# Kernel tuning notes

Hardware: AMD Instinct MI355X
Metric: run time of the kernel (lower is better)

The kernel has to match this reference:

```python
import jax, jax.numpy as jnp
import numpy as np

B, N, C = 1, 512, 256
LN_EPS = 1e-5


def mish(x):
    return x * jnp.tanh(jax.nn.softplus(x))


def layer_norm(x, g, b):
    mu = jnp.mean(x, axis=-1, keepdims=True)
    var = jnp.var(x, axis=-1, keepdims=True)
    return (x - mu) * jax.lax.rsqrt(var + LN_EPS) * g + b


def setup_inputs() -> dict:
    key = jax.random.key(0)
    ks = jax.random.split(key, 8)
    s = 1.0 / np.sqrt(C)
    lin = lambda k: jax.random.uniform(k, (C, C), jnp.float32, -s, s)
    return {
        "feat": jax.random.normal(ks[0], (B, N, C), jnp.float32),
        "Wq": lin(ks[1]), "bq": jnp.zeros((C,), jnp.float32),
        "ln_q_g": jnp.ones((C,), jnp.float32), "ln_q_b": jnp.zeros((C,), jnp.float32),
        "Wk": lin(ks[2]), "bk": jnp.zeros((C,), jnp.float32),
        "ln_k_g": jnp.ones((C,), jnp.float32), "ln_k_b": jnp.zeros((C,), jnp.float32),
        "Wv": lin(ks[3]), "bv": jnp.zeros((C,), jnp.float32),
        "W1": lin(ks[4]), "b1": jnp.zeros((C,), jnp.float32),
        "ln_w_g": jnp.ones((C,), jnp.float32), "ln_w_b": jnp.zeros((C,), jnp.float32),
        "W2": lin(ks[5]), "b2": jnp.zeros((C,), jnp.float32),
    }


def reference(feat, Wq, bq, ln_q_g, ln_q_b, Wk, bk, ln_k_g, ln_k_b,
              Wv, bv, W1, b1, ln_w_g, ln_w_b, W2, b2):
    # distribution: 1 where the row has any nonzero feature, else 0  -> [B, N, 1]
    dist = (jnp.sum(jnp.abs(feat), axis=-1, keepdims=True) > 0).astype(feat.dtype)

    q = mish(layer_norm(feat @ Wq + bq, ln_q_g, ln_q_b))  # [B, N, C]
    k = mish(layer_norm(feat @ Wk + bk, ln_k_g, ln_k_b))  # [B, N, C]
    v = feat @ Wv + bv                                     # [B, N, C]

    # relation_qk[b, i, j, c] = k[b, j, c] - q[b, i, c]
    rel = k[:, None, :, :] - q[:, :, None, :]              # [B, N, N, C]
    w = mish(layer_norm(rel @ W1 + b1, ln_w_g, ln_w_b)) @ W2 + b2  # [B, N, N, C]

    # weighted softmax over the key axis j (dim=-2), weights = dist -> [B,1,N,1]
    wts = dist[:, None, :, :]                              # [B, 1, N, 1]
    m = jnp.max(w, axis=-2, keepdims=True)
    e = jnp.exp(w - m) * wts
    attn = e / jnp.sum(e, axis=-2, keepdims=True)          # [B, N, N, C]

    mask = (dist * jnp.swapaxes(dist, -1, -2)) > 0         # [B, N, N]
    attn = attn * mask[..., None].astype(attn.dtype)

    return jnp.einsum('bijk,bjk->bik', attn, v)            # [B, N, C]
```

## Files before the change

### kernel.cpp

```cpp
#include <hip/hip_runtime.h>
#include <hip/hip_bf16.h>
#include <math.h>


#define N_ 512
#define C_ 256
#define NCHUNK 2
#define JPB (N_ / NCHUNK)
#define JT 32

typedef short s8v __attribute__((ext_vector_type(8)));
typedef short s4v __attribute__((ext_vector_type(4)));
typedef float f4v __attribute__((ext_vector_type(4)));
typedef float f16v __attribute__((ext_vector_type(16)));
typedef unsigned int u4v __attribute__((ext_vector_type(4)));

__device__ __forceinline__ unsigned short f2bf(float x) {
  union { __hip_bfloat16 h; unsigned short u; } cv;
  cv.h = __float2bfloat16(x);
  return cv.u;
}

__device__ __forceinline__ float mish_f(float x) {
  if (x > 25.f) return x;
  float y = 1.f + __expf(x);
  float y2 = y * y;
  return x * __fdividef(y2 - 1.f, y2 + 1.f);
}

__device__ __forceinline__ void blockReduce2(float& a, float& b, float* red) {
  #pragma unroll
  for (int m = 1; m < 64; m <<= 1) { a += __shfl_xor(a, m); b += __shfl_xor(b, m); }
  int lane = threadIdx.x & 63, w = threadIdx.x >> 6;
  if (lane == 0) { red[w] = a; red[4 + w] = b; }
  __syncthreads();
  a = red[0] + red[1] + red[2] + red[3];
  b = red[4] + red[5] + red[6] + red[7];
  __syncthreads();
}

__global__ void __launch_bounds__(256) prep_kernel(
    const float* __restrict__ feat,
    const float* __restrict__ Wq, const float* __restrict__ bq,
    const float* __restrict__ gq, const float* __restrict__ bgq,
    const float* __restrict__ Wk, const float* __restrict__ bk,
    const float* __restrict__ gk, const float* __restrict__ bgk,
    const float* __restrict__ Wv, const float* __restrict__ bv,
    const float* __restrict__ W1, const float* __restrict__ b1,
    float* __restrict__ dist, float* __restrict__ vout,
    float* __restrict__ Qp, float* __restrict__ Kp,
    float* __restrict__ muQ, float* __restrict__ s2Q,
    float* __restrict__ muK, float* __restrict__ s2K,
    unsigned short* __restrict__ Qb, unsigned short* __restrict__ Kb) {
  const int tid = threadIdx.x;
  const int r0 = blockIdx.x * 4;
  __shared__ float fL[4][C_];
  __shared__ float xq[4][C_];
  __shared__ float xk[4][C_];
  __shared__ float red[8];

  #pragma unroll
  for (int r = 0; r < 4; ++r) fL[r][tid] = feat[(r0 + r) * C_ + tid];
  __syncthreads();

  {
    float a = fabsf(fL[0][tid]), b = fabsf(fL[1][tid]);
    blockReduce2(a, b, red);
    if (tid == 0) { dist[r0 + 0] = a > 0.f ? 1.f : 0.f; dist[r0 + 1] = b > 0.f ? 1.f : 0.f; }
    a = fabsf(fL[2][tid]); b = fabsf(fL[3][tid]);
    blockReduce2(a, b, red);
    if (tid == 0) { dist[r0 + 2] = a > 0.f ? 1.f : 0.f; dist[r0 + 3] = b > 0.f ? 1.f : 0.f; }
  }

  float aq[4] = {0,0,0,0}, ak[4] = {0,0,0,0}, av[4] = {0,0,0,0};
  for (int cp = 0; cp < C_; ++cp) {
    float wq = Wq[cp * C_ + tid], wk = Wk[cp * C_ + tid], wv = Wv[cp * C_ + tid];
    #pragma unroll
    for (int r = 0; r < 4; ++r) {
      float f = fL[r][cp];
      aq[r] += f * wq; ak[r] += f * wk; av[r] += f * wv;
    }
  }
  {
    float bvv = bv[tid];
    #pragma unroll
    for (int r = 0; r < 4; ++r) vout[(r0 + r) * C_ + tid] = av[r] + bvv;
  }

  const float bqv = bq[tid], bkv = bk[tid];
  const float gqv = gq[tid], bgqv = bgq[tid], gkv = gk[tid], bgkv = bgk[tid];
  for (int r = 0; r < 4; ++r) {
    float qv = aq[r] + bqv, kv = ak[r] + bkv;
    float s1 = qv, s2 = qv * qv;
    blockReduce2(s1, s2, red);
    float mu = s1 * (1.f / C_);
    float rs = rsqrtf(s2 * (1.f / C_) - mu * mu + 1e-5f);
    xq[r][tid] = mish_f((qv - mu) * rs * gqv + bgqv);
    s1 = kv; s2 = kv * kv;
    blockReduce2(s1, s2, red);
    mu = s1 * (1.f / C_);
    rs = rsqrtf(s2 * (1.f / C_) - mu * mu + 1e-5f);
    xk[r][tid] = mish_f((kv - mu) * rs * gkv + bgkv);
  }
  __syncthreads();

  float pq[4] = {0,0,0,0}, pk[4] = {0,0,0,0};
  for (int cp = 0; cp < C_; ++cp) {
    float w1 = W1[cp * C_ + tid];
    #pragma unroll
    for (int r = 0; r < 4; ++r) { pq[r] += xq[r][cp] * w1; pk[r] += xk[r][cp] * w1; }
  }
  const float b1v = b1[tid];
  for (int r = 0; r < 4; ++r) {
    float qv2 = pq[r];
    float kv2 = pk[r] + b1v;
    Qp[(r0 + r) * C_ + tid] = qv2;
    Kp[(r0 + r) * C_ + tid] = kv2;
    Qb[(r0 + r) * C_ + tid] = f2bf(qv2);
    Kb[(r0 + r) * C_ + tid] = f2bf(kv2);
    float s1 = qv2, s2 = qv2 * qv2;
    blockReduce2(s1, s2, red);
    if (tid == 0) { muQ[r0 + r] = s1 * (1.f / C_); s2Q[r0 + r] = s2; }
    s1 = kv2; s2 = kv2 * kv2;
    blockReduce2(s1, s2, red);
    if (tid == 0) { muK[r0 + r] = s1 * (1.f / C_); s2K[r0 + r] = s2; }
  }
}

__global__ void __launch_bounds__(256) repack_kernel(
    const float* __restrict__ W2, unsigned short* __restrict__ W2f) {
  int idx = blockIdx.x * 256 + threadIdx.x;
  int e = idx & 7;
  int l = (idx >> 3) & 63;
  int ks = (idx >> 9) & 15;
  int w = idx >> 13;
  int k = ks * 16 + ((l >> 5) << 3) + e;
  int c = (w << 5) + (l & 31);
  W2f[idx] = f2bf(W2[k * C_ + c]);
}

__global__ void __launch_bounds__(256) gemmG_kernel(
    const unsigned short* __restrict__ Qb, const unsigned short* __restrict__ Kb,
    float* __restrict__ G) {
  const int tid = threadIdx.x;
  const int lane = tid & 63, wave = tid >> 6;
  const int bi = blockIdx.x >> 4, bj = blockIdx.x & 15;
  const int i0 = bi * 32 + (wave >> 1) * 16;
  const int j0 = bj * 32 + (wave & 1) * 16;
  const int jr = lane & 15, kg = lane >> 4;
  const unsigned short* qrow = Qb + (i0 + jr) * C_;
  const unsigned short* krow = Kb + (j0 + jr) * C_;
  f4v acc = (f4v){0.f, 0.f, 0.f, 0.f};
  #pragma unroll
  for (int ks = 0; ks < 8; ++ks) {
    const int kb = ks * 32 + kg * 4;
    s4v alo = *reinterpret_cast<const s4v*>(qrow + kb);
    s4v ahi = *reinterpret_cast<const s4v*>(qrow + kb + 16);
    s4v blo = *reinterpret_cast<const s4v*>(krow + kb);
    s4v bhi = *reinterpret_cast<const s4v*>(krow + kb + 16);
    s8v A, Bv;
    A[0]=alo[0];A[1]=alo[1];A[2]=alo[2];A[3]=alo[3];
    A[4]=ahi[0];A[5]=ahi[1];A[6]=ahi[2];A[7]=ahi[3];
    Bv[0]=blo[0];Bv[1]=blo[1];Bv[2]=blo[2];Bv[3]=blo[3];
    Bv[4]=bhi[0];Bv[5]=bhi[1];Bv[6]=bhi[2];Bv[7]=bhi[3];
    acc = __builtin_amdgcn_mfma_f32_16x16x32_bf16(A, Bv, acc, 0, 0, 0);
  }
  #pragma unroll
  for (int r = 0; r < 4; ++r)
    G[(i0 + kg * 4 + r) * N_ + j0 + jr] = acc[r];
}

__global__ void __launch_bounds__(512, 4) attn_kernel(
    const float* __restrict__ dist, const float* __restrict__ v,
    const float* __restrict__ Qp, const float* __restrict__ Kp,
    const float* __restrict__ muQ, const float* __restrict__ s2Q,
    const float* __restrict__ muK, const float* __restrict__ s2K,
    const float* __restrict__ G, const unsigned short* __restrict__ W2f,
    const float* __restrict__ gw, const float* __restrict__ bw,
    float* __restrict__ pden, float* __restrict__ pacc) {
  const int tid = threadIdx.x;
  const int i = blockIdx.x;
  const int chunk = blockIdx.y;
  const int j0 = chunk * JPB;
  const int lane = tid & 63, wave = tid >> 6;
  const int jg = tid >> 4, g = tid & 15;
  const int row = lane & 31, hi = lane >> 5;
  const int cw = (wave << 5) + row;

  __shared__ __align__(16) unsigned short T[JT * C_];
  __shared__ __align__(16) float qpP[80 * 4];
  __shared__ __align__(16) float gbL[144 * 4];
  __shared__ float muKL[JPB], s2KL[JPB], GL[JPB], distL[JPB];
  char* Tb = reinterpret_cast<char*>(T);

  if (tid < C_) {
    const int c = tid;
    qpP[(5 * (c >> 4) + ((c >> 2) & 3)) * 4 + (c & 3)] = Qp[i * C_ + c];
    const int pc = 9 * (c >> 4) + ((c & 15) >> 1);
    gbL[pc * 4 + (c & 1) * 2]     = gw[c];
    gbL[pc * 4 + (c & 1) * 2 + 1] = bw[c];
    muKL[tid] = muK[j0 + tid];
    s2KL[tid] = s2K[j0 + tid];
  } else {
    const int t = tid - C_;
    GL[t]    = G[i * N_ + j0 + t];
    distL[t] = dist[j0 + t];
  }

  s8v Bfr[16];
  #pragma unroll
  for (int ks = 0; ks < 16; ++ks)
    Bfr[ks] = *reinterpret_cast<const s8v*>(
        W2f + ((((wave << 4) + ks) * 64 + lane) << 3));

  const float muQ_i = muQ[i], s2Q_i = s2Q[i];

  float den = 0.f, accv = 0.f;
  __syncthreads();

  const int swz = (g & 7) << 6;
  const int wb0 = (((((g << 1)    ) << 5) + jg) << 4) ^ swz;
  const int wb1 = (((((g << 1) + 1) << 5) + jg) << 4) ^ swz;
  const f4v* qp4 = reinterpret_cast<const f4v*>(qpP) + 5 * g;
  const f4v* gb4 = reinterpret_cast<const f4v*>(gbL) + 9 * g;

  for (int jt = 0; jt < JPB / JT; ++jt) {
    const int jb = j0 + jt * JT;
    {
      const int jj = jt * JT + jg;
      const float muj = muKL[jj] - muQ_i;
      const float ex2 = (s2KL[jj] + s2Q_i - 2.f * GL[jj]) * (1.f / C_);
      const float rs = rsqrtf(fmaxf(ex2 - muj * muj, 0.f) + 1e-5f);
      const float* kpr = Kp + (j0 + jj) * C_ + (g << 4);
      u4v p0, p1;
      #pragma unroll
      for (int m = 0; m < 4; ++m) {
        f4v kk = *reinterpret_cast<const f4v*>(kpr + (m << 2));
        f4v qq = qp4[m];
        f4v ga  = gb4[2 * m];
        f4v gb_ = gb4[2 * m + 1];
        #pragma unroll
        for (int h = 0; h < 2; ++h) {
          f4v gg = h ? gb_ : ga;
          float x0 = kk[2 * h]     - qq[2 * h]     - muj;
          float x1 = kk[2 * h + 1] - qq[2 * h + 1] - muj;
          float a  = mish_f(fmaf(x0, rs * gg[0], gg[1]));
          float b2 = mish_f(fmaf(x1, rs * gg[2], gg[3]));
          unsigned pa = (__float_as_uint(a) + 0x8000u) >> 16;
          unsigned pb = (__float_as_uint(b2) + 0x8000u) & 0xFFFF0000u;
          unsigned pk = pa | pb;
          if (m < 2) p0[m * 2 + h] = pk; else p1[(m - 2) * 2 + h] = pk;
        }
      }
      *reinterpret_cast<u4v*>(Tb + wb0) = p0;
      *reinterpret_cast<u4v*>(Tb + wb1) = p1;
    }
    __syncthreads();

    f16v wv;
    #pragma unroll
    for (int r = 0; r < 16; ++r) wv[r] = 0.f;
    #pragma unroll
    for (int ks = 0; ks < 16; ++ks) {
      const int off = (((((ks << 1) + hi) << 5) + row) << 4) ^ ((ks & 7) << 6);
      s8v A = *reinterpret_cast<const s8v*>(Tb + off);
      wv = __builtin_amdgcn_mfma_f32_32x32x16_bf16(A, Bfr[ks], wv, 0, 0, 0);
    }

    #pragma unroll
    for (int r = 0; r < 16; ++r) {
      const int jj = (r & 3) + ((r >> 2) << 3) + (hi << 2);
      float e = __expf(fminf(wv[r], 60.f)) * distL[jt * JT + jj];
      den += e;
      accv += e * v[(jb + jj) * C_ + cw];
    }
    __syncthreads();
  }

  den  += __shfl_xor(den, 32);
  accv += __shfl_xor(accv, 32);
  if (lane < 32) {
    pden[(chunk * N_ + i) * C_ + cw] = den;
    pacc[(chunk * N_ + i) * C_ + cw] = accv;
  }
}

__global__ void __launch_bounds__(256) reduce_kernel(
    const float* __restrict__ dist,
    const float* __restrict__ pden, const float* __restrict__ pacc,
    float* __restrict__ out) {
  const int i = blockIdx.x, c = threadIdx.x;
  float den = 0.f, acc = 0.f;
  #pragma unroll
  for (int ch = 0; ch < NCHUNK; ++ch) {
    den += pden[(ch * N_ + i) * C_ + c];
    acc += pacc[(ch * N_ + i) * C_ + c];
  }
  float o = 0.f;
  if (dist[i] > 0.f && den > 0.f) o = acc / den;
  out[i * C_ + c] = o;
}

extern "C" void kernel_launch(void* const* d_in, const int* in_sizes, int n_in,
                              void* d_out, int out_size, void* d_ws, size_t ws_size,
                              hipStream_t stream) {
  const float* feat = (const float*)d_in[0];
  const float* Wq   = (const float*)d_in[1];
  const float* bq   = (const float*)d_in[2];
  const float* gq   = (const float*)d_in[3];
  const float* bgq  = (const float*)d_in[4];
  const float* Wk   = (const float*)d_in[5];
  const float* bk   = (const float*)d_in[6];
  const float* gk   = (const float*)d_in[7];
  const float* bgk  = (const float*)d_in[8];
  const float* Wv   = (const float*)d_in[9];
  const float* bv   = (const float*)d_in[10];
  const float* W1   = (const float*)d_in[11];
  const float* b1   = (const float*)d_in[12];
  const float* gw   = (const float*)d_in[13];
  const float* bw   = (const float*)d_in[14];
  const float* W2   = (const float*)d_in[15];

  char* ws = (char*)d_ws;
  float* dist = (float*)(ws + 0);
  float* muQ  = (float*)(ws + 2048);
  float* s2Q  = (float*)(ws + 4096);
  float* muK  = (float*)(ws + 6144);
  float* s2K  = (float*)(ws + 8192);
  float* v    = (float*)(ws + 0x010000);
  float* Qp   = (float*)(ws + 0x090000);
  float* Kp   = (float*)(ws + 0x110000);
  unsigned short* Qb  = (unsigned short*)(ws + 0x190000);
  unsigned short* Kb  = (unsigned short*)(ws + 0x1D0000);
  unsigned short* W2f = (unsigned short*)(ws + 0x210000);
  float* G    = (float*)(ws + 0x230000);
  float* pden = (float*)(ws + 0x330000);
  float* pacc = (float*)(ws + 0x430000);

  hipLaunchKernelGGL(prep_kernel, dim3(128), dim3(256), 0, stream,
                     feat, Wq, bq, gq, bgq, Wk, bk, gk, bgk, Wv, bv, W1, b1,
                     dist, v, Qp, Kp, muQ, s2Q, muK, s2K, Qb, Kb);
  hipLaunchKernelGGL(repack_kernel, dim3(256), dim3(256), 0, stream, W2, W2f);
  hipLaunchKernelGGL(gemmG_kernel, dim3(256), dim3(256), 0, stream, Qb, Kb, G);
  hipLaunchKernelGGL(attn_kernel, dim3(512, NCHUNK), dim3(512), 0, stream,
                     dist, v, Qp, Kp, muQ, s2Q, muK, s2K, G, W2f, gw, bw,
                     pden, pacc);
  hipLaunchKernelGGL(reduce_kernel, dim3(512), dim3(256), 0, stream,
                     dist, pden, pacc, (float*)d_out);
}
```

Baseline: 136.5 us.

## Double-buffer the relation tile so MFMA overlaps next tile's mish construction

The shared relation tile T becomes double-buffered. The first tile is built before the loop, and each iteration issues the MFMAs on the current buffer, then builds the next tile into the other buffer before the exp/accumulate epilogue. This leaves one barrier per iteration instead of two and lets MFMA execution overlap VALU transcendental work. In exchange, LDS use doubles (16KB to 32KB for T), which could limit occupancy at 4 blocks of 512 threads per CU, and register pressure rises from keeping the wv accumulator live across the tile build.

```diff
diff --git a/kernel.cpp b/kernel.cpp
--- a/kernel.cpp
+++ b/kernel.cpp
@@ -8,6 +8,7 @@
 #define NCHUNK 2
 #define JPB (N_ / NCHUNK)
 #define JT 32
+#define NT (JPB / JT)
 
 typedef short s8v __attribute__((ext_vector_type(8)));
 typedef short s4v __attribute__((ext_vector_type(4)));
@@ -187,7 +188,7 @@
   const int row = lane & 31, hi = lane >> 5;
   const int cw = (wave << 5) + row;
 
-  __shared__ __align__(16) unsigned short T[JT * C_];
+  __shared__ __align__(16) unsigned short T[2][JT * C_];
   __shared__ __align__(16) float qpP[80 * 4];
   __shared__ __align__(16) float gbL[144 * 4];
   __shared__ float muKL[JPB], s2KL[JPB], GL[JPB], distL[JPB];
@@ -216,7 +217,6 @@
   const float muQ_i = muQ[i], s2Q_i = s2Q[i];
 
   float den = 0.f, accv = 0.f;
-  __syncthreads();
 
   const int swz = (g & 7) << 6;
   const int wb0 = (((((g << 1)    ) << 5) + jg) << 4) ^ swz;
@@ -224,55 +224,71 @@
   const f4v* qp4 = reinterpret_cast<const f4v*>(qpP) + 5 * g;
   const f4v* gb4 = reinterpret_cast<const f4v*>(gbL) + 9 * g;
 
-  for (int jt = 0; jt < JPB / JT; ++jt) {
-    const int jb = j0 + jt * JT;
+  auto tphase = [&](int n, int buf) {
+    const int jj = n * JT + jg;
+    const float muj = muKL[jj] - muQ_i;
+    const float ex2 = (s2KL[jj] + s2Q_i - 2.f * GL[jj]) * (1.f / C_);
+    const float rs = rsqrtf(fmaxf(ex2 - muj * muj, 0.f) + 1e-5f);
+    const float* kpr = Kp + (j0 + jj) * C_ + (g << 4);
+    u4v p0, p1;
+    #pragma unroll
+    for (int m = 0; m < 4; ++m) {
+      f4v kk = *reinterpret_cast<const f4v*>(kpr + (m << 2));
+      f4v qq = qp4[m];
+      f4v ga  = gb4[2 * m];
+      f4v gb_ = gb4[2 * m + 1];
+      #pragma unroll
+      for (int h = 0; h < 2; ++h) {
+        f4v gg = h ? gb_ : ga;
+        float x0 = kk[2 * h]     - qq[2 * h]     - muj;
+        float x1 = kk[2 * h + 1] - qq[2 * h + 1] - muj;
+        float a  = mish_f(fmaf(x0, rs * gg[0], gg[1]));
+        float b2 = mish_f(fmaf(x1, rs * gg[2], gg[3]));
+        unsigned pa = (__float_as_uint(a) + 0x8000u) >> 16;
+        unsigned pb = (__float_as_uint(b2) + 0x8000u) & 0xFFFF0000u;
+        unsigned pk = pa | pb;
+        if (m < 2) p0[m * 2 + h] = pk; else p1[(m - 2) * 2 + h] = pk;
+      }
+    }
+    char* Tw = Tb + buf * (JT * C_ * 2);
+    *reinterpret_cast<u4v*>(Tw + wb0) = p0;
+    *reinterpret_cast<u4v*>(Tw + wb1) = p1;
+  };
+
+  __syncthreads();
+  tphase(0, 0);
+  __syncthreads();
+
+  for (int n = 0; n < NT; ++n) {
+    const int b = n & 1;
+    const char* Tr = Tb + b * (JT * C_ * 2);
+
+    f16v wv;
+    #pragma unroll
+    for (int r = 0; r < 16; ++r) wv[r] = 0.f;
+    #pragma unroll
+    for (int ks = 0; ks < 16; ++ks) {
+      const int off = (((((ks << 1) + hi) << 5) + row) << 4) ^ ((ks & 7) << 6);
+      s8v A = *reinterpret_cast<const s8v*>(Tr + off);
+      wv = __builtin_amdgcn_mfma_f32_32x32x16_bf16(A, Bfr[ks], wv, 0, 0, 0);
+    }
+
+    if (n + 1 < NT) tphase(n + 1, b ^ 1);
+
     {
-      const int jj = jt * JT + jg;
-      const float muj = muKL[jj] - muQ_i;
-      const float ex2 = (s2KL[jj] + s2Q_i - 2.f * GL[jj]) * (1.f / C_);
-      const float rs = rsqrtf(fmaxf(ex2 - muj * muj, 0.f) + 1e-5f);
-      const float* kpr = Kp + (j0 + jj) * C_ + (g << 4);
-      u4v p0, p1;
+      const int jb = j0 + n * JT + (hi << 2);
       #pragma unroll
-      for (int m = 0; m < 4; ++m) {
-        f4v kk = *reinterpret_cast<const f4v*>(kpr + (m << 2));
-        f4v qq = qp4[m];
-        f4v ga  = gb4[2 * m];
-        f4v gb_ = gb4[2 * m + 1];
+      for (int q = 0; q < 4; ++q) {
+        const float* vb = v + (jb + (q << 3)) * C_ + cw;
+        const float* dl = distL + n * JT + (hi << 2) + (q << 3);
         #pragma unroll
-        for (int h = 0; h < 2; ++h) {
-          f4v gg = h ? gb_ : ga;
-          float x0 = kk[2 * h]     - qq[2 * h]     - muj;
-          float x1 = kk[2 * h + 1] - qq[2 * h + 1] - muj;
-          float a  = mish_f(fmaf(x0, rs * gg[0], gg[1]));
-          float b2 = mish_f(fmaf(x1, rs * gg[2], gg[3]));
-          unsigned pa = (__float_as_uint(a) + 0x8000u) >> 16;
-          unsigned pb = (__float_as_uint(b2) + 0x8000u) & 0xFFFF0000u;
-          unsigned pk = pa | pb;
-          if (m < 2) p0[m * 2 + h] = pk; else p1[(m - 2) * 2 + h] = pk;
+        for (int s = 0; s < 4; ++s) {
+          const int r = (q << 2) + s;
+          float e = __expf(fminf(wv[r], 60.f)) * dl[s];
+          den += e;
+          accv += e * vb[s * C_];
         }
       }
-      *reinterpret_cast<u4v*>(Tb + wb0) = p0;
-      *reinterpret_cast<u4v*>(Tb + wb1) = p1;
-    }
-    __syncthreads();
-
-    f16v wv;
-    #pragma unroll
-    for (int r = 0; r < 16; ++r) wv[r] = 0.f;
-    #pragma unroll
-    for (int ks = 0; ks < 16; ++ks) {
-      const int off = (((((ks << 1) + hi) << 5) + row) << 4) ^ ((ks & 7) << 6);
-      s8v A = *reinterpret_cast<const s8v*>(Tb + off);
-      wv = __builtin_amdgcn_mfma_f32_32x32x16_bf16(A, Bfr[ks], wv, 0, 0, 0);
-    }
-
-    #pragma unroll
-    for (int r = 0; r < 16; ++r) {
-      const int jj = (r & 3) + ((r >> 2) << 3) + (hi << 2);
-      float e = __expf(fminf(wv[r], 60.f)) * distL[jt * JT + jj];
-      den += e;
-      accv += e * v[(jb + jj) * C_ + cw];
     }
     __syncthreads();
   }
```

Measured after the change: 205.8 us. +50.7%, slower.
